# Kernel tuning notes

Hardware: AMD Instinct MI355X
Metric: run time of the kernel (lower is better)

Reference implementation:

```python
import jax, jax.numpy as jnp
import numpy as np

B, R, S, D, K = 4096, 49, 50, 512, 100

def setup_inputs() -> dict:
    key = jax.random.key(0)
    ks = jax.random.split(key, 10)
    return {
        "ifeature": jax.random.normal(ks[0], (B, R, D), dtype=jnp.float32),
        "tfeature_h": jax.random.normal(ks[1], (B, S, D), dtype=jnp.float32),
        "w_Vi_0": jax.random.normal(ks[2], (D, K), dtype=jnp.float32) * 0.05,
        "w_Vt_0": jax.random.normal(ks[3], (D, K), dtype=jnp.float32) * 0.05,
        "w_Pi_0": jax.random.normal(ks[4], (2 * K, 1), dtype=jnp.float32) * 0.05,
        "b_Pi_0": jnp.zeros((R,), dtype=jnp.float32),
        "w_Vi_1": jax.random.normal(ks[5], (D, K), dtype=jnp.float32) * 0.05,
        "w_Vt_1": jax.random.normal(ks[6], (D, K), dtype=jnp.float32) * 0.05,
        "w_Pi_1": jax.random.normal(ks[7], (2 * K, 1), dtype=jnp.float32) * 0.05,
        "b_Pi_1": jnp.zeros((S,), dtype=jnp.float32),
    }

def reference(ifeature, tfeature_h, w_Vi_0, w_Vt_0, w_Pi_0, b_Pi_0,
              w_Vi_1, w_Vt_1, w_Pi_1, b_Pi_1):
    # ---- pass 0: attend over image regions, conditioned on mean text feature
    tfeature = jnp.mean(tfeature_h, axis=1)                      # [B, D]
    wVi0 = jnp.einsum('brd,dk->brk', ifeature, w_Vi_0)           # [B, R, K]
    wVt0 = (tfeature @ w_Vt_0)[:, None, :]                       # [B, 1, K] -> broadcast over R
    Hi = jnp.tanh(jnp.concatenate(
        [wVi0, jnp.broadcast_to(wVt0, wVi0.shape)], axis=-1))    # [B, R, 2K]
    scores_i = jnp.squeeze(Hi @ w_Pi_0, axis=-1) + b_Pi_0        # [B, R]
    Pi = jax.nn.softmax(scores_i, axis=-1)                       # [B, R]
    Vi = jnp.einsum('br,brd->bd', Pi, ifeature)                  # [B, D]
    # ---- pass 1: attend over text positions, conditioned on attended image
    wVi1 = (Vi @ w_Vi_1)[:, None, :]                             # [B, 1, K]
    wVt1 = jnp.einsum('bsd,dk->bsk', tfeature_h, w_Vt_1)         # [B, S, K]
    Ht = jnp.tanh(jnp.concatenate(
        [jnp.broadcast_to(wVi1, wVt1.shape), wVt1], axis=-1))    # [B, S, 2K]
    scores_t = jnp.squeeze(Ht @ w_Pi_1, axis=-1) + b_Pi_1        # [B, S]
    Pt = jax.nn.softmax(scores_t, axis=-1)                       # [B, S]
    Vt = jnp.einsum('bs,bsd->bd', Pt, tfeature_h)                # [B, D]
    return Vi + Vt
```

## Files before the change

### kernel.cpp

```cpp
#include <hip/hip_runtime.h>
#include <math.h>

#define NB 4096
#define NR 49
#define NS 50
#define ND 512
#define NK 100
#define NT 7
#define KSTEPS 16
#define FRAGS (NT * KSTEPS * 64 * 8)

typedef __attribute__((ext_vector_type(8))) short short8;
typedef __attribute__((ext_vector_type(4))) float f32x4;

__device__ __forceinline__ unsigned short f32_bf16(float f) {
    union { float f; unsigned u; } x; x.f = f;
    return (unsigned short)((x.u + 0x7fffu + ((x.u >> 16) & 1u)) >> 16);
}
__device__ __forceinline__ unsigned cvt_pk_bf16(float lo, float hi) {
    unsigned r;
    asm("v_cvt_pk_bf16_f32 %0, %1, %2" : "=v"(r) : "v"(lo), "v"(hi));
    return r;
}
__device__ __forceinline__ float fast_tanh(float x) {
    const float ax = fabsf(x);
    const float e = __expf(2.f * ax);
    const float r = 1.f - 2.f / (e + 1.f);
    return copysignf(r, x);
}
__device__ __forceinline__ void load_lds16(const float* g, float* l) {
    __builtin_amdgcn_global_load_lds(
        (const __attribute__((address_space(1))) unsigned int*)(const void*)g,
        (__attribute__((address_space(3))) unsigned int*)(void*)l, 16, 0, 0);
}
#define FENCE() asm volatile("" ::: "memory")
#define BARR()  do { FENCE(); __builtin_amdgcn_s_barrier(); FENCE(); } while (0)
#define WAITV(N) asm volatile("s_waitcnt vmcnt(" #N ")" ::: "memory")

__global__ void preswz_kernel(const float* __restrict__ w0, const float* __restrict__ w1,
                              unsigned short* __restrict__ ws)
{
    const int l  = threadIdx.x;
    const int gk = blockIdx.x & 15;
    const int t  = blockIdx.x >> 4;
    const int m  = blockIdx.y;
    const float* W = m ? w1 : w0;
    const int col = t * 16 + (l & 15);
    const int k0  = gk * 32 + (l >> 4) * 8;
    unsigned short* o = ws + (size_t)m * FRAGS + ((size_t)(t * 16 + gk) * 64 + l) * 8;
#pragma unroll
    for (int j = 0; j < 8; ++j) {
        float v = (col < NK) ? W[(size_t)(k0 + j) * NK + col] : 0.f;
        o[j] = f32_bf16(v);
    }
}

struct SM {
    float bufA[50 * 128];
    float bufB[50 * 128];
    float part[8][64];
    float P[64];
};

__global__ __launch_bounds__(512, 4) void coattn_main(
    const float* __restrict__ ifeat, const float* __restrict__ tfeat,
    const float* __restrict__ wPi0, const float* __restrict__ bPi0,
    const float* __restrict__ wPi1, const float* __restrict__ bPi1,
    const unsigned short* __restrict__ wsW, float* __restrict__ out)
{
    __shared__ SM sm;
    const int pass = blockIdx.x & 1;
    const int b    = blockIdx.x >> 1;
    const int tid  = threadIdx.x;

    const float* feat = pass ? (tfeat + (size_t)b * NS * ND) : (ifeat + (size_t)b * NR * ND);
    const int nrows  = pass ? NS : NR;
    const int nclamp = nrows - 1;
    const unsigned short* wsR = wsW + (size_t)pass * FRAGS;
    const float* wPiRow = pass ? (wPi1 + NK) : wPi0;
    const float* bvec   = pass ? bPi1 : bPi0;

    const int lane = tid & 63, wid = tid >> 6;
    const int colg = lane & 15, g = lane >> 4;
    const int q  = wid >> 1;
    const int mh = wid & 1;
    const int t0 = q * 2;
    const int two = (q < 3);

    int arow_[2], aswz_[2];
#pragma unroll
    for (int rl = 0; rl < 2; ++rl) {
        const int r0 = (mh * 2 + rl) * 16 + colg;
        arow_[rl] = (r0 < nclamp) ? r0 : nclamp;
        aswz_[rl] = arow_[rl] & 7;
    }
    const unsigned short* wl0 = wsR + ((size_t)t0 * 16 * 64 + lane) * 8;
    const unsigned short* wl1 = wl0 + (size_t)16 * 64 * 8;

#define ISSUE(CP, BUF)                                                          \
    do {                                                                        \
        _Pragma("unroll") for (int s = 0; s < 3; ++s) {                         \
            const int j = wid + (s << 3);                                       \
            const int row = 2 * j + (lane >> 5);                                \
            const int grow = (row < nrows) ? row : nclamp;                      \
            const int c16 = lane & 31;                                          \
            load_lds16(feat + (grow << 9) + ((CP) << 7) + ((c16 ^ (row & 7)) << 2), \
                       sm.BUF + j * 256);                                       \
        }                                                                       \
        if (wid == 0) {                                                         \
            const int row = 48 + (lane >> 5);                                   \
            const int grow = (row < nrows) ? row : nclamp;                      \
            const int c16 = lane & 31;                                          \
            load_lds16(feat + (grow << 9) + ((CP) << 7) + ((c16 ^ (row & 7)) << 2), \
                       sm.BUF + 24 * 256);                                      \
        }                                                                       \
    } while (0)
#define WAITC() do { if (wid == 0) { WAITV(4); } else { WAITV(3); } } while (0)

    f32x4 acc[2][2];
#pragma unroll
    for (int rl = 0; rl < 2; ++rl)
#pragma unroll
        for (int tl = 0; tl < 2; ++tl) acc[rl][tl] = f32x4{0.f, 0.f, 0.f, 0.f};

#define GEMMP(LB, CP)                                                           \
    do {                                                                        \
        _Pragma("unroll") for (int ksl = 0; ksl < 4; ++ksl) {                   \
            const int ks = (CP) * 4 + ksl;                                      \
            const short8 wf0 = *reinterpret_cast<const short8*>(wl0 + ks * 512); \
            short8 wf1 = {};                                                    \
            if (two) wf1 = *reinterpret_cast<const short8*>(wl1 + ks * 512);    \
            _Pragma("unroll") for (int rl = 0; rl < 2; ++rl) {                  \
                const int c16 = (ksl << 3) + (g << 1);                          \
                const float4 fa = *reinterpret_cast<const float4*>(             \
                    &(LB)[arow_[rl] * 128 + ((c16 ^ aswz_[rl]) << 2)]);         \
                const float4 fb = *reinterpret_cast<const float4*>(             \
                    &(LB)[arow_[rl] * 128 + (((c16 + 1) ^ aswz_[rl]) << 2)]);   \
                uint4 ap;                                                       \
                ap.x = cvt_pk_bf16(fa.x, fa.y); ap.y = cvt_pk_bf16(fa.z, fa.w); \
                ap.z = cvt_pk_bf16(fb.x, fb.y); ap.w = cvt_pk_bf16(fb.z, fb.w); \
                const short8 a = *reinterpret_cast<const short8*>(&ap);         \
                acc[rl][0] = __builtin_amdgcn_mfma_f32_16x16x32_bf16(a, wf0, acc[rl][0], 0, 0, 0); \
                if (two)                                                        \
                    acc[rl][1] = __builtin_amdgcn_mfma_f32_16x16x32_bf16(a, wf1, acc[rl][1], 0, 0, 0); \
            }                                                                   \
        }                                                                       \
    } while (0)

    ISSUE(0, bufA);
    ISSUE(1, bufB);
    WAITC(); BARR();
    GEMMP(sm.bufA, 0);
    BARR();
    ISSUE(2, bufA);
    WAITC(); BARR();
    GEMMP(sm.bufB, 1);
    BARR();
    ISSUE(3, bufB);
    WAITC(); BARR();
    GEMMP(sm.bufA, 2);
    WAITV(0); BARR();
    GEMMP(sm.bufB, 3);

    {
        const int c0 = (t0 + 0) * 16 + colg;
        const int c1 = (t0 + 1) * 16 + colg;
        const float w0 = (c0 < NK) ? wPiRow[c0] : 0.f;
        const float w1 = (two && c1 < NK) ? wPiRow[c1] : 0.f;
        float sp[2][4];
#pragma unroll
        for (int rl = 0; rl < 2; ++rl)
#pragma unroll
            for (int i = 0; i < 4; ++i) {
                float v = fast_tanh(acc[rl][0][i]) * w0;
                if (two) v += fast_tanh(acc[rl][1][i]) * w1;
                sp[rl][i] = v;
            }
#pragma unroll
        for (int off = 1; off < 16; off <<= 1)
#pragma unroll
            for (int rl = 0; rl < 2; ++rl)
#pragma unroll
                for (int i = 0; i < 4; ++i)
                    sp[rl][i] += __shfl_xor(sp[rl][i], off);
        if (colg == 0) {
#pragma unroll
            for (int rl = 0; rl < 2; ++rl)
#pragma unroll
                for (int i = 0; i < 4; ++i)
                    sm.part[wid][(mh * 2 + rl) * 16 + g * 4 + i] = sp[rl][i];
        }
    }
    __syncthreads();

    if (tid < 64) {
        const int hb = (tid >= 32) ? 1 : 0;
        float v = (tid < nrows) ? bvec[tid] : 0.f;
#pragma unroll
        for (int qq = 0; qq < 4; ++qq) v += sm.part[2 * qq + hb][tid];
        v = (tid < nrows) ? v : -3.0e38f;
        float mx = v;
#pragma unroll
        for (int off = 32; off; off >>= 1) mx = fmaxf(mx, __shfl_xor(mx, off));
        const float e = (tid < nrows) ? __expf(v - mx) : 0.f;
        float su = e;
#pragma unroll
        for (int off = 32; off; off >>= 1) su += __shfl_xor(su, off);
        sm.P[tid] = e / su;
    }
    __syncthreads();

    {
        float v = 0.f;
        const float* fp = feat + tid;
        if (pass == 0) {
#pragma unroll
            for (int r = 0; r < NR; ++r) v += sm.P[r] * fp[(size_t)r << 9];
        } else {
#pragma unroll
            for (int r = 0; r < NS; ++r) v += sm.P[r] * fp[(size_t)r << 9];
        }
        atomicAdd(&out[(size_t)b * ND + tid], v);
    }
#undef ISSUE
#undef WAITC
#undef GEMMP
}

extern "C" void kernel_launch(void* const* d_in, const int* in_sizes, int n_in,
                              void* d_out, int out_size, void* d_ws, size_t ws_size,
                              hipStream_t stream) {
    const float* ifeat = (const float*)d_in[0];
    const float* tfeat = (const float*)d_in[1];
    const float* wVi0  = (const float*)d_in[2];
    const float* wPi0  = (const float*)d_in[4];
    const float* bPi0  = (const float*)d_in[5];
    const float* wVt1  = (const float*)d_in[7];
    const float* wPi1  = (const float*)d_in[8];
    const float* bPi1  = (const float*)d_in[9];
    float* outp = (float*)d_out;
    unsigned short* wsW = (unsigned short*)d_ws;

    hipMemsetAsync(outp, 0, (size_t)NB * ND * sizeof(float), stream);
    hipLaunchKernelGGL(preswz_kernel, dim3(NT * KSTEPS, 2), dim3(64), 0, stream,
                       wVi0, wVt1, wsW);
    hipLaunchKernelGGL(coattn_main, dim3(2 * NB), dim3(512), 0, stream,
                       ifeat, tfeat, wPi0, bPi0, wPi1, bPi1, wsW, outp);
}
```

Measured before the change: 311.6 us.

## Load GEMM A-operand directly from global memory, dropping LDS staging buffers

Removes the double-buffered global-to-LDS async staging of the feature tile and the barriers around it. Each wave now reads its A fragments directly from global memory with float4 loads inside a fully unrolled k-loop. This shrinks shared memory use, which could allow more resident blocks, and removes the barrier stalls. The cost is that rows are fetched redundantly by the waves that share them, and loads become strided per lane, so performance relies on L1/L2 cache hits.

Result: slower. 490.2 us (+57.3%).

```diff
diff --git a/kernel.cpp b/kernel.cpp
--- a/kernel.cpp
+++ b/kernel.cpp
@@ -28,14 +28,6 @@
     const float r = 1.f - 2.f / (e + 1.f);
     return copysignf(r, x);
 }
-__device__ __forceinline__ void load_lds16(const float* g, float* l) {
-    __builtin_amdgcn_global_load_lds(
-        (const __attribute__((address_space(1))) unsigned int*)(const void*)g,
-        (__attribute__((address_space(3))) unsigned int*)(void*)l, 16, 0, 0);
-}
-#define FENCE() asm volatile("" ::: "memory")
-#define BARR()  do { FENCE(); __builtin_amdgcn_s_barrier(); FENCE(); } while (0)
-#define WAITV(N) asm volatile("s_waitcnt vmcnt(" #N ")" ::: "memory")
 
 __global__ void preswz_kernel(const float* __restrict__ w0, const float* __restrict__ w1,
                               unsigned short* __restrict__ ws)
@@ -56,8 +48,6 @@
 }
 
 struct SM {
-    float bufA[50 * 128];
-    float bufB[50 * 128];
     float part[8][64];
     float P[64];
 };
@@ -87,35 +77,15 @@
     const int t0 = q * 2;
     const int two = (q < 3);
 
-    int arow_[2], aswz_[2];
+    const float* fA[2];
 #pragma unroll
     for (int rl = 0; rl < 2; ++rl) {
         const int r0 = (mh * 2 + rl) * 16 + colg;
-        arow_[rl] = (r0 < nclamp) ? r0 : nclamp;
-        aswz_[rl] = arow_[rl] & 7;
+        const int arow = (r0 < nclamp) ? r0 : nclamp;
+        fA[rl] = feat + ((size_t)arow << 9) + (g << 3);
     }
     const unsigned short* wl0 = wsR + ((size_t)t0 * 16 * 64 + lane) * 8;
     const unsigned short* wl1 = wl0 + (size_t)16 * 64 * 8;
-
-#define ISSUE(CP, BUF)                                                          \
-    do {                                                                        \
-        _Pragma("unroll") for (int s = 0; s < 3; ++s) {                         \
-            const int j = wid + (s << 3);                                       \
-            const int row = 2 * j + (lane >> 5);                                \
-            const int grow = (row < nrows) ? row : nclamp;                      \
-            const int c16 = lane & 31;                                          \
-            load_lds16(feat + (grow << 9) + ((CP) << 7) + ((c16 ^ (row & 7)) << 2), \
-                       sm.BUF + j * 256);                                       \
-        }                                                                       \
-        if (wid == 0) {                                                         \
-            const int row = 48 + (lane >> 5);                                   \
-            const int grow = (row < nrows) ? row : nclamp;                      \
-            const int c16 = lane & 31;                                          \
-            load_lds16(feat + (grow << 9) + ((CP) << 7) + ((c16 ^ (row & 7)) << 2), \
-                       sm.BUF + 24 * 256);                                      \
-        }                                                                       \
-    } while (0)
-#define WAITC() do { if (wid == 0) { WAITV(4); } else { WAITV(3); } } while (0)
 
     f32x4 acc[2][2];
 #pragma unroll
@@ -123,44 +93,24 @@
 #pragma unroll
         for (int tl = 0; tl < 2; ++tl) acc[rl][tl] = f32x4{0.f, 0.f, 0.f, 0.f};
 
-#define GEMMP(LB, CP)                                                           \
-    do {                                                                        \
-        _Pragma("unroll") for (int ksl = 0; ksl < 4; ++ksl) {                   \
-            const int ks = (CP) * 4 + ksl;                                      \
-            const short8 wf0 = *reinterpret_cast<const short8*>(wl0 + ks * 512); \
-            short8 wf1 = {};                                                    \
-            if (two) wf1 = *reinterpret_cast<const short8*>(wl1 + ks * 512);    \
-            _Pragma("unroll") for (int rl = 0; rl < 2; ++rl) {                  \
-                const int c16 = (ksl << 3) + (g << 1);                          \
-                const float4 fa = *reinterpret_cast<const float4*>(             \
-                    &(LB)[arow_[rl] * 128 + ((c16 ^ aswz_[rl]) << 2)]);         \
-                const float4 fb = *reinterpret_cast<const float4*>(             \
-                    &(LB)[arow_[rl] * 128 + (((c16 + 1) ^ aswz_[rl]) << 2)]);   \
-                uint4 ap;                                                       \
-                ap.x = cvt_pk_bf16(fa.x, fa.y); ap.y = cvt_pk_bf16(fa.z, fa.w); \
-                ap.z = cvt_pk_bf16(fb.x, fb.y); ap.w = cvt_pk_bf16(fb.z, fb.w); \
-                const short8 a = *reinterpret_cast<const short8*>(&ap);         \
-                acc[rl][0] = __builtin_amdgcn_mfma_f32_16x16x32_bf16(a, wf0, acc[rl][0], 0, 0, 0); \
-                if (two)                                                        \
-                    acc[rl][1] = __builtin_amdgcn_mfma_f32_16x16x32_bf16(a, wf1, acc[rl][1], 0, 0, 0); \
-            }                                                                   \
-        }                                                                       \
-    } while (0)
-
-    ISSUE(0, bufA);
-    ISSUE(1, bufB);
-    WAITC(); BARR();
-    GEMMP(sm.bufA, 0);
-    BARR();
-    ISSUE(2, bufA);
-    WAITC(); BARR();
-    GEMMP(sm.bufB, 1);
-    BARR();
-    ISSUE(3, bufB);
-    WAITC(); BARR();
-    GEMMP(sm.bufA, 2);
-    WAITV(0); BARR();
-    GEMMP(sm.bufB, 3);
+#pragma unroll
+    for (int ks = 0; ks < KSTEPS; ++ks) {
+        const short8 wf0 = *reinterpret_cast<const short8*>(wl0 + ks * 512);
+        short8 wf1 = {};
+        if (two) wf1 = *reinterpret_cast<const short8*>(wl1 + ks * 512);
+#pragma unroll
+        for (int rl = 0; rl < 2; ++rl) {
+            const float4 fa = *reinterpret_cast<const float4*>(fA[rl] + ks * 32);
+            const float4 fb = *reinterpret_cast<const float4*>(fA[rl] + ks * 32 + 4);
+            uint4 ap;
+            ap.x = cvt_pk_bf16(fa.x, fa.y); ap.y = cvt_pk_bf16(fa.z, fa.w);
+            ap.z = cvt_pk_bf16(fb.x, fb.y); ap.w = cvt_pk_bf16(fb.z, fb.w);
+            const short8 a = *reinterpret_cast<const short8*>(&ap);
+            acc[rl][0] = __builtin_amdgcn_mfma_f32_16x16x32_bf16(a, wf0, acc[rl][0], 0, 0, 0);
+            if (two)
+                acc[rl][1] = __builtin_amdgcn_mfma_f32_16x16x32_bf16(a, wf1, acc[rl][1], 0, 0, 0);
+        }
+    }
 
     {
         const int c0 = (t0 + 0) * 16 + colg;
@@ -222,9 +172,6 @@
         }
         atomicAdd(&out[(size_t)b * ND + tid], v);
     }
-#undef ISSUE
-#undef WAITC
-#undef GEMMP
 }
 
 extern "C" void kernel_launch(void* const* d_in, const int* in_sizes, int n_in,
```

## Make main kernel persistent over 16 batches with cross-batch chunk prefetch

Applied to the files above, without the earlier changes.

Each block now handles 16 consecutive batch elements instead of one, looping over them. The double-buffered LDS chunk pipeline continues across batch boundaries, so the next batch's first feature chunks load while the current batch runs its softmax and weighted-sum tail. This is meant to hide the per-block prologue and load latency and cut block launch overhead. The grid shrinks to 512 blocks, which may leave CUs underfilled at 4 blocks per CU and serializes work per block.

New measurement: 596.8 us. 91.5% more time.

```diff
diff --git a/kernel.cpp b/kernel.cpp
--- a/kernel.cpp
+++ b/kernel.cpp
@@ -8,6 +8,9 @@
 #define NK 100
 #define NT 7
 #define KSTEPS 16
+#define NBATCH 16
+#define NGRP (NB / NBATCH)
+#define NCHUNK (4 * NBATCH)
 #define FRAGS (NT * KSTEPS * 64 * 8)
 
 typedef __attribute__((ext_vector_type(8))) short short8;
@@ -36,6 +39,7 @@
 #define FENCE() asm volatile("" ::: "memory")
 #define BARR()  do { FENCE(); __builtin_amdgcn_s_barrier(); FENCE(); } while (0)
 #define WAITV(N) asm volatile("s_waitcnt vmcnt(" #N ")" ::: "memory")
+#define LGK0()  asm volatile("s_waitcnt lgkmcnt(0)" ::: "memory")
 
 __global__ void preswz_kernel(const float* __restrict__ w0, const float* __restrict__ w1,
                               unsigned short* __restrict__ ws)
@@ -70,12 +74,12 @@
 {
     __shared__ SM sm;
     const int pass = blockIdx.x & 1;
-    const int b    = blockIdx.x >> 1;
+    const int grp  = blockIdx.x >> 1;
     const int tid  = threadIdx.x;
 
-    const float* feat = pass ? (tfeat + (size_t)b * NS * ND) : (ifeat + (size_t)b * NR * ND);
     const int nrows  = pass ? NS : NR;
     const int nclamp = nrows - 1;
+    const float* featB = (pass ? tfeat : ifeat) + (size_t)grp * NBATCH * nrows * ND;
     const unsigned short* wsR = wsW + (size_t)pass * FRAGS;
     const float* wPiRow = pass ? (wPi1 + NK) : wPi0;
     const float* bvec   = pass ? bPi1 : bPi0;
@@ -97,31 +101,27 @@
     const unsigned short* wl0 = wsR + ((size_t)t0 * 16 * 64 + lane) * 8;
     const unsigned short* wl1 = wl0 + (size_t)16 * 64 * 8;
 
-#define ISSUE(CP, BUF)                                                          \
+#define ISSUE_CH(N, BUF)                                                        \
     do {                                                                        \
+        const float* fsrc = featB + (size_t)((N) >> 2) * nrows * ND             \
+                                  + (((N) & 3) << 7);                           \
         _Pragma("unroll") for (int s = 0; s < 3; ++s) {                         \
             const int j = wid + (s << 3);                                       \
             const int row = 2 * j + (lane >> 5);                                \
             const int grow = (row < nrows) ? row : nclamp;                      \
             const int c16 = lane & 31;                                          \
-            load_lds16(feat + (grow << 9) + ((CP) << 7) + ((c16 ^ (row & 7)) << 2), \
+            load_lds16(fsrc + (grow << 9) + ((c16 ^ (row & 7)) << 2),           \
                        sm.BUF + j * 256);                                       \
         }                                                                       \
         if (wid == 0) {                                                         \
             const int row = 48 + (lane >> 5);                                   \
             const int grow = (row < nrows) ? row : nclamp;                      \
             const int c16 = lane & 31;                                          \
-            load_lds16(feat + (grow << 9) + ((CP) << 7) + ((c16 ^ (row & 7)) << 2), \
+            load_lds16(fsrc + (grow << 9) + ((c16 ^ (row & 7)) << 2),           \
                        sm.BUF + 24 * 256);                                      \
         }                                                                       \
     } while (0)
 #define WAITC() do { if (wid == 0) { WAITV(4); } else { WAITV(3); } } while (0)
-
-    f32x4 acc[2][2];
-#pragma unroll
-    for (int rl = 0; rl < 2; ++rl)
-#pragma unroll
-        for (int tl = 0; tl < 2; ++tl) acc[rl][tl] = f32x4{0.f, 0.f, 0.f, 0.f};
 
 #define GEMMP(LB, CP)                                                           \
     do {                                                                        \
@@ -147,82 +147,97 @@
         }                                                                       \
     } while (0)
 
-    ISSUE(0, bufA);
-    ISSUE(1, bufB);
-    WAITC(); BARR();
-    GEMMP(sm.bufA, 0);
-    BARR();
-    ISSUE(2, bufA);
-    WAITC(); BARR();
-    GEMMP(sm.bufB, 1);
-    BARR();
-    ISSUE(3, bufB);
-    WAITC(); BARR();
-    GEMMP(sm.bufA, 2);
-    WAITV(0); BARR();
-    GEMMP(sm.bufB, 3);
-
-    {
-        const int c0 = (t0 + 0) * 16 + colg;
-        const int c1 = (t0 + 1) * 16 + colg;
-        const float w0 = (c0 < NK) ? wPiRow[c0] : 0.f;
-        const float w1 = (two && c1 < NK) ? wPiRow[c1] : 0.f;
-        float sp[2][4];
+    ISSUE_CH(0, bufA);
+    ISSUE_CH(1, bufB);
+
+#pragma unroll 1
+    for (int i = 0; i < NBATCH; ++i) {
+        f32x4 acc[2][2];
 #pragma unroll
         for (int rl = 0; rl < 2; ++rl)
 #pragma unroll
-            for (int i = 0; i < 4; ++i) {
-                float v = fast_tanh(acc[rl][0][i]) * w0;
-                if (two) v += fast_tanh(acc[rl][1][i]) * w1;
-                sp[rl][i] = v;
+            for (int tl = 0; tl < 2; ++tl) acc[rl][tl] = f32x4{0.f, 0.f, 0.f, 0.f};
+
+        WAITC(); BARR();
+        GEMMP(sm.bufA, 0);
+        BARR();
+        { const int n = 4 * i + 2; if (n < NCHUNK) ISSUE_CH(n, bufA); }
+        WAITC(); BARR();
+        GEMMP(sm.bufB, 1);
+        BARR();
+        { const int n = 4 * i + 3; if (n < NCHUNK) ISSUE_CH(n, bufB); }
+        WAITC(); BARR();
+        GEMMP(sm.bufA, 2);
+        BARR();
+        { const int n = 4 * i + 4; if (n < NCHUNK) ISSUE_CH(n, bufA); }
+        if (i == NBATCH - 1) { WAITV(0); } else { WAITC(); }
+        BARR();
+        GEMMP(sm.bufB, 3);
+        BARR();
+        { const int n = 4 * i + 5; if (n < NCHUNK) ISSUE_CH(n, bufB); }
+
+        {
+            const int c0 = (t0 + 0) * 16 + colg;
+            const int c1 = (t0 + 1) * 16 + colg;
+            const float w0 = (c0 < NK) ? wPiRow[c0] : 0.f;
+            const float w1 = (two && c1 < NK) ? wPiRow[c1] : 0.f;
+            float sp[2][4];
+#pragma unroll
+            for (int rl = 0; rl < 2; ++rl)
+#pragma unroll
+                for (int ii = 0; ii < 4; ++ii) {
+                    float v = fast_tanh(acc[rl][0][ii]) * w0;
+                    if (two) v += fast_tanh(acc[rl][1][ii]) * w1;
+                    sp[rl][ii] = v;
+                }
+#pragma unroll
+            for (int off = 1; off < 16; off <<= 1)
+#pragma unroll
+                for (int rl = 0; rl < 2; ++rl)
+#pragma unroll
+                    for (int ii = 0; ii < 4; ++ii)
+                        sp[rl][ii] += __shfl_xor(sp[rl][ii], off);
+            if (colg == 0) {
+#pragma unroll
+                for (int rl = 0; rl < 2; ++rl)
+#pragma unroll
+                    for (int ii = 0; ii < 4; ++ii)
+                        sm.part[wid][(mh * 2 + rl) * 16 + g * 4 + ii] = sp[rl][ii];
             }
-#pragma unroll
-        for (int off = 1; off < 16; off <<= 1)
-#pragma unroll
-            for (int rl = 0; rl < 2; ++rl)
-#pragma unroll
-                for (int i = 0; i < 4; ++i)
-                    sp[rl][i] += __shfl_xor(sp[rl][i], off);
-        if (colg == 0) {
-#pragma unroll
-            for (int rl = 0; rl < 2; ++rl)
-#pragma unroll
-                for (int i = 0; i < 4; ++i)
-                    sm.part[wid][(mh * 2 + rl) * 16 + g * 4 + i] = sp[rl][i];
+        }
+        LGK0(); BARR();
+
+        if (tid < 64) {
+            const int hb = (tid >= 32) ? 1 : 0;
+            float v = (tid < nrows) ? bvec[tid] : 0.f;
+#pragma unroll
+            for (int qq = 0; qq < 4; ++qq) v += sm.part[2 * qq + hb][tid];
+            v = (tid < nrows) ? v : -3.0e38f;
+            float mx = v;
+#pragma unroll
+            for (int off = 32; off; off >>= 1) mx = fmaxf(mx, __shfl_xor(mx, off));
+            const float e = (tid < nrows) ? __expf(v - mx) : 0.f;
+            float su = e;
+#pragma unroll
+            for (int off = 32; off; off >>= 1) su += __shfl_xor(su, off);
+            sm.P[tid] = e / su;
+        }
+        LGK0(); BARR();
+
+        {
+            const float* fi = featB + (size_t)i * nrows * ND + tid;
+            float v = 0.f;
+            if (pass == 0) {
+#pragma unroll
+                for (int r = 0; r < NR; ++r) v += sm.P[r] * fi[(size_t)r << 9];
+            } else {
+#pragma unroll
+                for (int r = 0; r < NS; ++r) v += sm.P[r] * fi[(size_t)r << 9];
+            }
+            atomicAdd(&out[(size_t)(grp * NBATCH + i) * ND + tid], v);
         }
     }
-    __syncthreads();
-
-    if (tid < 64) {
-        const int hb = (tid >= 32) ? 1 : 0;
-        float v = (tid < nrows) ? bvec[tid] : 0.f;
-#pragma unroll
-        for (int qq = 0; qq < 4; ++qq) v += sm.part[2 * qq + hb][tid];
-        v = (tid < nrows) ? v : -3.0e38f;
-        float mx = v;
-#pragma unroll
-        for (int off = 32; off; off >>= 1) mx = fmaxf(mx, __shfl_xor(mx, off));
-        const float e = (tid < nrows) ? __expf(v - mx) : 0.f;
-        float su = e;
-#pragma unroll
-        for (int off = 32; off; off >>= 1) su += __shfl_xor(su, off);
-        sm.P[tid] = e / su;
-    }
-    __syncthreads();
-
-    {
-        float v = 0.f;
-        const float* fp = feat + tid;
-        if (pass == 0) {
-#pragma unroll
-            for (int r = 0; r < NR; ++r) v += sm.P[r] * fp[(size_t)r << 9];
-        } else {
-#pragma unroll
-            for (int r = 0; r < NS; ++r) v += sm.P[r] * fp[(size_t)r << 9];
-        }
-        atomicAdd(&out[(size_t)b * ND + tid], v);
-    }
-#undef ISSUE
+#undef ISSUE_CH
 #undef WAITC
 #undef GEMMP
 }
@@ -244,6 +259,6 @@
     hipMemsetAsync(outp, 0, (size_t)NB * ND * sizeof(float), stream);
     hipLaunchKernelGGL(preswz_kernel, dim3(NT * KSTEPS, 2), dim3(64), 0, stream,
                        wVi0, wVt1, wsW);
-    hipLaunchKernelGGL(coattn_main, dim3(2 * NB), dim3(512), 0, stream,
+    hipLaunchKernelGGL(coattn_main, dim3(2 * NGRP), dim3(512), 0, stream,
                        ifeat, tfeat, wPi0, bPi0, wPi1, bPi1, wsW, outp);
 }
```
